# Optimization experiments

Measured on AMD Instinct MI355X. Metric: run time of the kernel, lower is better.

## Reference

```python
import math
import jax, jax.numpy as jnp
import numpy as np

B, H, D, N, M = 4, 8, 64, 8192, 256
EPS = 1e-6


def sample_orthogonal_random_vectors(num_rows, num_cols, seed=0):
    """Faithful port of FavorAttention.sample_orthogonal_random_vectors."""
    rng = np.random.default_rng(seed)
    num_blocks = math.ceil(num_rows / num_cols)
    unstructured = rng.standard_normal((num_blocks, num_cols, num_cols)).astype(np.float32)
    norm = np.linalg.norm(unstructured, axis=-1).reshape(-1, 1)
    q, _ = np.linalg.qr(unstructured)                 # reduced QR per block
    q = np.transpose(q, (0, 2, 1)).reshape(-1, num_cols)
    q = q[:num_rows, :] * norm[:num_rows, :]
    return jnp.asarray(q, dtype=jnp.float32)


def setup_inputs() -> dict:
    key = jax.random.key(0)
    kq, kk, kv = jax.random.split(key, 3)
    return {
        "query": jax.random.normal(kq, (B, H, D, N), dtype=jnp.float32),
        "key": jax.random.normal(kk, (B, H, D, N), dtype=jnp.float32),
        "value": jax.random.normal(kv, (B, H, D, N), dtype=jnp.float32),
        "projection_matrix": sample_orthogonal_random_vectors(M, D),
    }


def randomized_kernel(x, proj, is_query, eps=EPS):
    """FAVOR+ positive softmax features. x: [B,H,D,N] -> phi: [B,H,M,N]."""
    d = x.shape[2]
    data_normalizer = d ** -0.25
    ratio = proj.shape[0] ** -0.5
    # projected: [B,H,M,N]
    u = jnp.einsum('md,bhdn->bhmn', proj, x) * data_normalizer
    # ||x||^2 / (2*sqrt(d)) per token: [B,H,1,N]
    diag = jnp.sum(x * x, axis=2, keepdims=True) * (data_normalizer ** 2) * 0.5
    if is_query:
        stab = jnp.max(u, axis=2, keepdims=True)            # per-token max over features
    else:
        stab = jnp.max(u, axis=(2, 3), keepdims=True)       # global max per (b,h)
    return ratio * (jnp.exp(u - diag - stab) + eps)


def reference(query, key, value, projection_matrix):
    q_phi = randomized_kernel(query, projection_matrix, is_query=True)    # [B,H,M,N]
    k_phi = randomized_kernel(key, projection_matrix, is_query=False)     # [B,H,M,N]
    # kv = key @ value^T over sequence: [B,H,M,D]
    kv = jnp.einsum('bhmn,bhdn->bhmd', k_phi, value)
    key_norm = jnp.sum(k_phi, axis=3)                                     # [B,H,M]
    out = jnp.einsum('bhmn,bhmd->bhnd', q_phi, kv)                        # [B,H,N,D]
    out_norm = jnp.einsum('bhmn,bhm->bhn', q_phi, key_norm)[..., None]    # [B,H,N,1]
    out = out / out_norm
    return jnp.swapaxes(out, 2, 3)                                        # [B,H,D,N]


if __name__ == '__main__':
    o = reference(**setup_inputs())
    print(o.shape, o.dtype)
```

## Files before the change

kernel.cpp:

```cpp
#include <hip/hip_runtime.h>


typedef short s16x8 __attribute__((ext_vector_type(8)));
typedef float f32x4 __attribute__((ext_vector_type(4)));

#define Dv 64
#define Nv 8192
#define Mv 256
#define BHv 32
#define SPL 16
#define NSPL (Nv / SPL)
#define NCH (NSPL / 64)

#define DNRM 0.3535533905932738f
#define EPSV 1e-6f
#define KSTAB 15.0f

#define BARRIER_RAW()                                        \
    do {                                                     \
        asm volatile("s_waitcnt lgkmcnt(0)" ::: "memory");   \
        __builtin_amdgcn_s_barrier();                        \
        __builtin_amdgcn_sched_barrier(0);                   \
    } while (0)

#define OFF_SD 0
#define OFF_T (OFF_SD + BHv * Dv)
#define OFF_SGM (OFF_T + BHv)
#define OFF_SVP (OFF_SGM + BHv * SPL * 4)
#define OFF_KNP (OFF_SVP + BHv * SPL * 64)
#define OFF_KNF (OFF_KNP + BHv * SPL * Mv)
#define OFF_KVP (OFF_KNF + BHv * Mv)
#define OFF_KVT (OFF_KVP + BHv * SPL * Mv * Dv)
#define ZERO_FLOATS (OFF_SGM)

__device__ __forceinline__ unsigned short f2b(float x) {
    return __builtin_bit_cast(unsigned short, (__bf16)x);
}

__device__ __forceinline__ s16x8 load_pfrag(const float* __restrict__ proj, int m,
                                            int kc, int q) {
    const float* p = proj + m * 64 + kc * 32 + q * 8;
    s16x8 r;
#pragma unroll
    for (int j = 0; j < 8; ++j) r[j] = (short)f2b(p[j]);
    return r;
}

__global__ __launch_bounds__(256, 2) void favor_kv(const float* __restrict__ key,
                                                   const float* __restrict__ value,
                                                   const float* __restrict__ proj,
                                                   float* __restrict__ ws) {
    __shared__ __align__(16) unsigned short KT[64][72];
    __shared__ __align__(16) unsigned short VL[64][72];
    __shared__ __align__(16) unsigned short PH[256][40];
    __shared__ __align__(16) float dred[16][64];
    __shared__ __align__(16) float dgl[64];
    const int tid = threadIdx.x;
    const int w = tid >> 6, l = tid & 63, c = l & 15, q = l >> 4;
    const int g = tid >> 4, cs = tid & 15;
    const int s = blockIdx.x, bh = blockIdx.y;
    const float* kp = key + (size_t)bh * Dv * Nv;
    const float* vp = value + (size_t)bh * Dv * Nv;

    s16x8 P[4][2];
#pragma unroll
    for (int mt = 0; mt < 4; ++mt)
#pragma unroll
        for (int kc = 0; kc < 2; ++kc)
            P[mt][kc] = load_pfrag(proj, (4 * w + mt) * 16 + c, kc, q);

    f32x4 kva[4][4];
#pragma unroll
    for (int mt = 0; mt < 4; ++mt)
#pragma unroll
        for (int dt = 0; dt < 4; ++dt) kva[mt][dt] = (f32x4){0.f, 0.f, 0.f, 0.f};
    float kn[4] = {0.f, 0.f, 0.f, 0.f};
    float sv[4] = {0.f, 0.f, 0.f, 0.f};
    float tmax = -3.0e38f;

    float4 kk[4], vv[4];
    {
        const int n0 = s * NSPL;
#pragma unroll
        for (int di = 0; di < 4; ++di) {
            kk[di] = *(const float4*)&kp[(4 * g + di) * Nv + n0 + 4 * cs];
            vv[di] = *(const float4*)&vp[(4 * g + di) * Nv + n0 + 4 * cs];
        }
    }

    for (int ch = 0; ch < NCH; ++ch) {
        if (ch) BARRIER_RAW();
#pragma unroll
        for (int j = 0; j < 4; ++j) {
            const float k0 = ((const float*)&kk[0])[j];
            const float k1 = ((const float*)&kk[1])[j];
            const float k2 = ((const float*)&kk[2])[j];
            const float k3 = ((const float*)&kk[3])[j];
            *(short4*)&KT[4 * cs + j][4 * g] =
                make_short4((short)f2b(k0), (short)f2b(k1), (short)f2b(k2),
                            (short)f2b(k3));
            dred[g][4 * cs + j] = (k0 * k0 + k1 * k1) + (k2 * k2 + k3 * k3);
        }
#pragma unroll
        for (int di = 0; di < 4; ++di) {
            *(short4*)&VL[4 * g + di][4 * cs] = make_short4(
                (short)f2b(vv[di].x), (short)f2b(vv[di].y),
                (short)f2b(vv[di].z), (short)f2b(vv[di].w));
            sv[di] += (vv[di].x + vv[di].y) + (vv[di].z + vv[di].w);
        }
        if (ch + 1 < NCH) {
            const int n1 = s * NSPL + (ch + 1) * 64;
#pragma unroll
            for (int di = 0; di < 4; ++di) {
                kk[di] = *(const float4*)&kp[(4 * g + di) * Nv + n1 + 4 * cs];
                vv[di] = *(const float4*)&vp[(4 * g + di) * Nv + n1 + 4 * cs];
            }
        }
        BARRIER_RAW();
        if (tid < 64) {
            float ds = 0.f;
#pragma unroll
            for (int gg = 0; gg < 16; ++gg) ds += dred[gg][tid];
            dgl[tid] = ds * 0.0625f + KSTAB;
        }
        BARRIER_RAW();
#pragma unroll
        for (int h = 0; h < 2; ++h) {
#pragma unroll
            for (int nt2 = 0; nt2 < 2; ++nt2) {
                const int nt = 2 * h + nt2;
                const s16x8 a0 = *(const s16x8*)&KT[nt * 16 + c][q * 8];
                const s16x8 a1 = *(const s16x8*)&KT[nt * 16 + c][32 + q * 8];
                const float4 dg = *(const float4*)&dgl[nt * 16 + q * 4];
#pragma unroll
                for (int mt = 0; mt < 4; ++mt) {
                    f32x4 u = {0.f, 0.f, 0.f, 0.f};
                    u = __builtin_amdgcn_mfma_f32_16x16x32_bf16(a0, P[mt][0], u, 0, 0, 0);
                    u = __builtin_amdgcn_mfma_f32_16x16x32_bf16(a1, P[mt][1], u, 0, 0, 0);
                    tmax = fmaxf(tmax, fmaxf(fmaxf(u[0], u[1]), fmaxf(u[2], u[3])));
                    const float e0 = __expf(__builtin_fmaf(u[0], DNRM, -dg.x));
                    const float e1 = __expf(__builtin_fmaf(u[1], DNRM, -dg.y));
                    const float e2 = __expf(__builtin_fmaf(u[2], DNRM, -dg.z));
                    const float e3 = __expf(__builtin_fmaf(u[3], DNRM, -dg.w));
                    kn[mt] += (e0 + e1) + (e2 + e3);
                    *(short4*)&PH[(4 * w + mt) * 16 + c][nt2 * 16 + q * 4] =
                        make_short4((short)f2b(e0), (short)f2b(e1),
                                    (short)f2b(e2), (short)f2b(e3));
                }
            }
            s16x8 bf[4];
#pragma unroll
            for (int dt = 0; dt < 4; ++dt)
                bf[dt] = *(const s16x8*)&VL[dt * 16 + c][h * 32 + q * 8];
#pragma unroll
            for (int mt = 0; mt < 4; ++mt) {
                const s16x8 a = *(const s16x8*)&PH[(4 * w + mt) * 16 + c][q * 8];
#pragma unroll
                for (int dt = 0; dt < 4; ++dt)
                    kva[mt][dt] = __builtin_amdgcn_mfma_f32_16x16x32_bf16(
                        a, bf[dt], kva[mt][dt], 0, 0, 0);
            }
        }
    }
#pragma unroll
    for (int off = 1; off < 64; off <<= 1)
        tmax = fmaxf(tmax, __shfl_xor(tmax, off, 64));
    if (l == 0) ws[OFF_SGM + (bh * SPL + s) * 4 + w] = tmax * DNRM;
    float* kvp = ws + OFF_KVP + (size_t)(bh * SPL + s) * Mv * Dv;
#pragma unroll
    for (int mt = 0; mt < 4; ++mt) {
        const int mrow = (4 * w + mt) * 16 + 4 * q;
#pragma unroll
        for (int dt = 0; dt < 4; ++dt) {
            const int dcol = dt * 16 + c;
#pragma unroll
            for (int r = 0; r < 4; ++r)
                kvp[(size_t)(mrow + r) * Dv + dcol] = kva[mt][dt][r];
        }
    }
#pragma unroll
    for (int mt = 0; mt < 4; ++mt) {
        kn[mt] += __shfl_xor(kn[mt], 16, 64);
        kn[mt] += __shfl_xor(kn[mt], 32, 64);
    }
    if (q == 0) {
        float* knp = ws + OFF_KNP + (bh * SPL + s) * Mv;
#pragma unroll
        for (int mt = 0; mt < 4; ++mt) knp[(4 * w + mt) * 16 + c] = kn[mt];
    }
    __syncthreads();
    float* sp = &dred[0][0];
#pragma unroll
    for (int di = 0; di < 4; ++di) sp[(4 * g + di) * 16 + cs] = sv[di];
    __syncthreads();
    if (tid < 64) {
        float t2 = 0.f;
#pragma unroll
        for (int j = 0; j < 16; ++j) t2 += sp[tid * 16 + j];
        ws[OFF_SVP + (bh * SPL + s) * 64 + tid] = t2;
    }
}

__global__ __launch_bounds__(256) void favor_kvred(float* __restrict__ ws) {
    __shared__ float sAl;
    __shared__ float svl[64];
    const int t = threadIdx.x, f = blockIdx.x, bh = blockIdx.y;
    const int flat = f * 1024 + t * 4;
    const int m = flat >> 6, d0 = flat & 63;
    if (t < 64) {
        float v = ws[OFF_SGM + bh * 64 + t];
#pragma unroll
        for (int off = 1; off < 64; off <<= 1)
            v = fmaxf(v, __shfl_xor(v, off, 64));
        if (t == 0) sAl = __expf(KSTAB - v);
    } else if (t < 128) {
        const int d = t - 64;
        float x = 0.f;
#pragma unroll
        for (int s2 = 0; s2 < SPL; ++s2)
            x += ws[OFF_SVP + (bh * SPL + s2) * 64 + d];
        svl[d] = x;
    }
    __syncthreads();
    const float al = sAl;
    float4 acc = make_float4(0.f, 0.f, 0.f, 0.f);
    for (int s2 = 0; s2 < SPL; ++s2) {
        const float4 v =
            *(const float4*)&ws[OFF_KVP + ((size_t)(bh * SPL + s2) << 14) + flat];
        acc.x += v.x; acc.y += v.y; acc.z += v.z; acc.w += v.w;
    }
    acc.x = acc.x * al + EPSV * svl[d0 + 0];
    acc.y = acc.y * al + EPSV * svl[d0 + 1];
    acc.z = acc.z * al + EPSV * svl[d0 + 2];
    acc.w = acc.w * al + EPSV * svl[d0 + 3];
    unsigned short* kvT = (unsigned short*)(ws + OFF_KVT);
    kvT[(bh * 64 + d0 + 0) * 256 + m] = f2b(acc.x);
    kvT[(bh * 64 + d0 + 1) * 256 + m] = f2b(acc.y);
    kvT[(bh * 64 + d0 + 2) * 256 + m] = f2b(acc.z);
    kvT[(bh * 64 + d0 + 3) * 256 + m] = f2b(acc.w);
    atomicAdd(&ws[OFF_SD + bh * 64 + d0 + 0], acc.x);
    atomicAdd(&ws[OFF_SD + bh * 64 + d0 + 1], acc.y);
    atomicAdd(&ws[OFF_SD + bh * 64 + d0 + 2], acc.z);
    atomicAdd(&ws[OFF_SD + bh * 64 + d0 + 3], acc.w);
    if (t < 16) {
        const int mm = f * 16 + t;
        float kk = 0.f;
        for (int s2 = 0; s2 < SPL; ++s2)
            kk += ws[OFF_KNP + (bh * SPL + s2) * Mv + mm];
        const float knf = kk * al + EPSV * (float)Nv;
        ws[OFF_KNF + bh * Mv + mm] = knf;
        atomicAdd(&ws[OFF_T + bh], knf);
    }
}

__global__ __launch_bounds__(256, 2) void favor_out(const float* __restrict__ query,
                                                    const float* __restrict__ proj,
                                                    const float* __restrict__ ws,
                                                    float* __restrict__ out) {
    __shared__ __align__(16) unsigned short PHT[64][264];
    __shared__ __align__(16) unsigned short KVL[64][264];
    __shared__ float npart[4][64];
    __shared__ float knl[256];
    __shared__ float cw[4][64];
    __shared__ float dql[64];
    __shared__ float Sl[64];
    __shared__ float Ts;
    unsigned short (*QT)[72] = (unsigned short (*)[72]) & PHT[0][0];
    float (*dred)[64] = (float (*)[64])((char*)&PHT[0][0] + 9216);
    const int tid = threadIdx.x;
    const int w = tid >> 6, l = tid & 63, c = l & 15, q = l >> 4;
    const int g = tid >> 4, cs = tid & 15;
    const int nb = blockIdx.x, bh = blockIdx.y;
    const int n0 = nb * 64;
    const float* qp = query + (size_t)bh * Dv * Nv;
    const uint4* kvg = (const uint4*)((const unsigned short*)(ws + OFF_KVT) +
                                      (size_t)bh * 64 * 256);

    float4 qq[4];
#pragma unroll
    for (int di = 0; di < 4; ++di)
        qq[di] = *(const float4*)&qp[(4 * g + di) * Nv + n0 + 4 * cs];
    uint4 kvr[8];
#pragma unroll
    for (int i = 0; i < 8; ++i) kvr[i] = kvg[i * 256 + tid];

#pragma unroll
    for (int j = 0; j < 4; ++j) {
        const float v0 = ((const float*)&qq[0])[j];
        const float v1 = ((const float*)&qq[1])[j];
        const float v2 = ((const float*)&qq[2])[j];
        const float v3 = ((const float*)&qq[3])[j];
        *(short4*)&QT[4 * cs + j][4 * g] =
            make_short4((short)f2b(v0), (short)f2b(v1), (short)f2b(v2),
                        (short)f2b(v3));
        dred[g][4 * cs + j] = (v0 * v0 + v1 * v1) + (v2 * v2 + v3 * v3);
    }
#pragma unroll
    for (int i = 0; i < 8; ++i) {
        const int j = i * 256 + tid;
        *(uint4*)&KVL[j >> 5][(j & 31) * 8] = kvr[i];
    }
    knl[tid] = ws[OFF_KNF + bh * Mv + tid];
    if (tid < 64) Sl[tid] = ws[OFF_SD + bh * 64 + tid];
    if (tid == 0) Ts = ws[OFF_T + bh];

    s16x8 P[4][2];
#pragma unroll
    for (int mt = 0; mt < 4; ++mt)
#pragma unroll
        for (int kc = 0; kc < 2; ++kc)
            P[mt][kc] = load_pfrag(proj, (4 * w + mt) * 16 + c, kc, q);
    __syncthreads();

    if (tid < 64) {
        float dsum = 0.f;
#pragma unroll
        for (int gg = 0; gg < 16; ++gg) dsum += dred[gg][tid];
        dql[tid] = dsum * 0.0625f;
    }
    float knr[4][4];
#pragma unroll
    for (int mt = 0; mt < 4; ++mt) {
        const int mb = (4 * w + mt) * 16 + 4 * q;
#pragma unroll
        for (int r = 0; r < 4; ++r) knr[mt][r] = knl[mb + r];
    }

    f32x4 u[4][4];
#pragma unroll
    for (int mt = 0; mt < 4; ++mt)
#pragma unroll
        for (int nt = 0; nt < 4; ++nt) u[mt][nt] = (f32x4){0.f, 0.f, 0.f, 0.f};
#pragma unroll
    for (int nt = 0; nt < 4; ++nt) {
        const s16x8 b0 = *(const s16x8*)&QT[nt * 16 + c][q * 8];
        const s16x8 b1 = *(const s16x8*)&QT[nt * 16 + c][32 + q * 8];
#pragma unroll
        for (int mt = 0; mt < 4; ++mt) {
            u[mt][nt] =
                __builtin_amdgcn_mfma_f32_16x16x32_bf16(P[mt][0], b0, u[mt][nt], 0, 0, 0);
            u[mt][nt] =
                __builtin_amdgcn_mfma_f32_16x16x32_bf16(P[mt][1], b1, u[mt][nt], 0, 0, 0);
        }
    }
    __syncthreads();
#pragma unroll
    for (int nt = 0; nt < 4; ++nt) {
        const float dq = dql[nt * 16 + c];
        float np = 0.f;
        float vm = -3.4e38f;
#pragma unroll
        for (int mt = 0; mt < 4; ++mt) {
            vm = fmaxf(vm, fmaxf(fmaxf(u[mt][nt][0], u[mt][nt][1]),
                                 fmaxf(u[mt][nt][2], u[mt][nt][3])));
            const float e0 = __expf(__builtin_fmaf(u[mt][nt][0], DNRM, -dq));
            const float e1 = __expf(__builtin_fmaf(u[mt][nt][1], DNRM, -dq));
            const float e2 = __expf(__builtin_fmaf(u[mt][nt][2], DNRM, -dq));
            const float e3 = __expf(__builtin_fmaf(u[mt][nt][3], DNRM, -dq));
            const int mb = (4 * w + mt) * 16 + 4 * q;
            np += e0 * knr[mt][0] + e1 * knr[mt][1] + e2 * knr[mt][2] +
                  e3 * knr[mt][3];
            *(short4*)&PHT[nt * 16 + c][mb] = make_short4(
                (short)f2b(e0), (short)f2b(e1), (short)f2b(e2), (short)f2b(e3));
        }
        np += __shfl_xor(np, 16, 64);
        np += __shfl_xor(np, 32, 64);
        vm = fmaxf(vm, __shfl_xor(vm, 16, 64));
        vm = fmaxf(vm, __shfl_xor(vm, 32, 64));
        if (q == 0) {
            npart[w][nt * 16 + c] = np;
            cw[w][nt * 16 + c] = vm;
        }
    }
    __syncthreads();
    f32x4 acc[4];
#pragma unroll
    for (int dt = 0; dt < 4; ++dt) acc[dt] = (f32x4){0.f, 0.f, 0.f, 0.f};
#pragma unroll
    for (int kc = 0; kc < 8; ++kc) {
        const s16x8 a = *(const s16x8*)&PHT[w * 16 + c][kc * 32 + q * 8];
#pragma unroll
        for (int dt = 0; dt < 4; ++dt) {
            const s16x8 b = *(const s16x8*)&KVL[dt * 16 + c][kc * 32 + q * 8];
            acc[dt] = __builtin_amdgcn_mfma_f32_16x16x32_bf16(a, b, acc[dt], 0, 0, 0);
        }
    }
    __syncthreads();
    float* ot = (float*)&PHT[0][0];
    float rn[4], gm[4];
#pragma unroll
    for (int r = 0; r < 4; ++r) {
        const int nl = w * 16 + 4 * q + r;
        const float npsum = (npart[0][nl] + npart[1][nl]) +
                            (npart[2][nl] + npart[3][nl]);
        const float st =
            fmaxf(fmaxf(cw[0][nl], cw[1][nl]), fmaxf(cw[2][nl], cw[3][nl]));
        const float gamma = EPSV * __expf(st * DNRM);
        gm[r] = gamma;
        rn[r] = 1.0f / (npsum + gamma * Ts);
    }
#pragma unroll
    for (int dt = 0; dt < 4; ++dt)
#pragma unroll
        for (int r = 0; r < 4; ++r)
            ot[(dt * 16 + c) * 68 + (w * 16 + 4 * q + r)] =
                (acc[dt][r] + gm[r] * Sl[dt * 16 + c]) * rn[r];
    __syncthreads();
    float* op = out + (size_t)bh * Dv * Nv;
    {
        const int d = tid >> 2, ng = (tid & 3) * 16;
#pragma unroll
        for (int i = 0; i < 4; ++i) {
            const float4 v = *(const float4*)&ot[d * 68 + ng + i * 4];
            *(float4*)&op[d * Nv + n0 + ng + i * 4] = v;
        }
    }
}

extern "C" void kernel_launch(void* const* d_in, const int* in_sizes, int n_in,
                              void* d_out, int out_size, void* d_ws, size_t ws_size,
                              hipStream_t stream) {
    const float* q = (const float*)d_in[0];
    const float* k = (const float*)d_in[1];
    const float* v = (const float*)d_in[2];
    const float* proj = (const float*)d_in[3];
    float* ws = (float*)d_ws;
    float* out = (float*)d_out;

    hipMemsetAsync(ws, 0, (size_t)ZERO_FLOATS * sizeof(float), stream);
    favor_kv<<<dim3(SPL, 32), 256, 0, stream>>>(k, v, proj, ws);
    favor_kvred<<<dim3(16, 32), 256, 0, stream>>>(ws);
    favor_out<<<dim3(Nv / 64, 32), 256, 0, stream>>>(q, proj, ws, out);
}
```

Baseline: 324.8 us.

## Process two token tiles per output block and drop memset and atomics

The output kernel now covers 128 tokens per block in two passes. This amortizes the staging of the bf16 kv matrix, the key norms and the projection fragments, and prefetches the second query tile early. The column sums of kv and the total key norm are now recomputed in each block from the staged data, which removes the global atomics and the workspace memset launch. The cost is fewer blocks (half the grid), a serial 256-element sum in a few threads, and Sl now being a sum of bf16-rounded values.

```diff
diff --git a/kernel.cpp b/kernel.cpp
--- a/kernel.cpp
+++ b/kernel.cpp
@@ -23,18 +23,19 @@
         __builtin_amdgcn_sched_barrier(0);                   \
     } while (0)
 
-#define OFF_SD 0
-#define OFF_T (OFF_SD + BHv * Dv)
-#define OFF_SGM (OFF_T + BHv)
+#define OFF_SGM 0
 #define OFF_SVP (OFF_SGM + BHv * SPL * 4)
 #define OFF_KNP (OFF_SVP + BHv * SPL * 64)
 #define OFF_KNF (OFF_KNP + BHv * SPL * Mv)
 #define OFF_KVP (OFF_KNF + BHv * Mv)
 #define OFF_KVT (OFF_KVP + BHv * SPL * Mv * Dv)
-#define ZERO_FLOATS (OFF_SGM)
 
 __device__ __forceinline__ unsigned short f2b(float x) {
     return __builtin_bit_cast(unsigned short, (__bf16)x);
+}
+__device__ __forceinline__ float b2f(unsigned short u) {
+    const unsigned int v = ((unsigned int)u) << 16;
+    return __builtin_bit_cast(float, v);
 }
 
 __device__ __forceinline__ s16x8 load_pfrag(const float* __restrict__ proj, int m,
@@ -238,18 +239,12 @@
     kvT[(bh * 64 + d0 + 1) * 256 + m] = f2b(acc.y);
     kvT[(bh * 64 + d0 + 2) * 256 + m] = f2b(acc.z);
     kvT[(bh * 64 + d0 + 3) * 256 + m] = f2b(acc.w);
-    atomicAdd(&ws[OFF_SD + bh * 64 + d0 + 0], acc.x);
-    atomicAdd(&ws[OFF_SD + bh * 64 + d0 + 1], acc.y);
-    atomicAdd(&ws[OFF_SD + bh * 64 + d0 + 2], acc.z);
-    atomicAdd(&ws[OFF_SD + bh * 64 + d0 + 3], acc.w);
     if (t < 16) {
         const int mm = f * 16 + t;
         float kk = 0.f;
         for (int s2 = 0; s2 < SPL; ++s2)
             kk += ws[OFF_KNP + (bh * SPL + s2) * Mv + mm];
-        const float knf = kk * al + EPSV * (float)Nv;
-        ws[OFF_KNF + bh * Mv + mm] = knf;
-        atomicAdd(&ws[OFF_T + bh], knf);
+        ws[OFF_KNF + bh * Mv + mm] = kk * al + EPSV * (float)Nv;
     }
 }
 
@@ -264,32 +259,35 @@
     __shared__ float cw[4][64];
     __shared__ float dql[64];
     __shared__ float Sl[64];
-    __shared__ float Ts;
+    __shared__ float Tsh;
     unsigned short (*QT)[72] = (unsigned short (*)[72]) & PHT[0][0];
     float (*dred)[64] = (float (*)[64])((char*)&PHT[0][0] + 9216);
     const int tid = threadIdx.x;
     const int w = tid >> 6, l = tid & 63, c = l & 15, q = l >> 4;
     const int g = tid >> 4, cs = tid & 15;
     const int nb = blockIdx.x, bh = blockIdx.y;
-    const int n0 = nb * 64;
+    const int n0 = nb * 128;
     const float* qp = query + (size_t)bh * Dv * Nv;
     const uint4* kvg = (const uint4*)((const unsigned short*)(ws + OFF_KVT) +
                                       (size_t)bh * 64 * 256);
 
-    float4 qq[4];
+    float4 qqA[4], qqB[4];
 #pragma unroll
     for (int di = 0; di < 4; ++di)
-        qq[di] = *(const float4*)&qp[(4 * g + di) * Nv + n0 + 4 * cs];
+        qqA[di] = *(const float4*)&qp[(4 * g + di) * Nv + n0 + 4 * cs];
     uint4 kvr[8];
 #pragma unroll
     for (int i = 0; i < 8; ++i) kvr[i] = kvg[i * 256 + tid];
+#pragma unroll
+    for (int di = 0; di < 4; ++di)
+        qqB[di] = *(const float4*)&qp[(4 * g + di) * Nv + n0 + 64 + 4 * cs];
 
 #pragma unroll
     for (int j = 0; j < 4; ++j) {
-        const float v0 = ((const float*)&qq[0])[j];
-        const float v1 = ((const float*)&qq[1])[j];
-        const float v2 = ((const float*)&qq[2])[j];
-        const float v3 = ((const float*)&qq[3])[j];
+        const float v0 = ((const float*)&qqA[0])[j];
+        const float v1 = ((const float*)&qqA[1])[j];
+        const float v2 = ((const float*)&qqA[2])[j];
+        const float v3 = ((const float*)&qqA[3])[j];
         *(short4*)&QT[4 * cs + j][4 * g] =
             make_short4((short)f2b(v0), (short)f2b(v1), (short)f2b(v2),
                         (short)f2b(v3));
@@ -301,8 +299,6 @@
         *(uint4*)&KVL[j >> 5][(j & 31) * 8] = kvr[i];
     }
     knl[tid] = ws[OFF_KNF + bh * Mv + tid];
-    if (tid < 64) Sl[tid] = ws[OFF_SD + bh * 64 + tid];
-    if (tid == 0) Ts = ws[OFF_T + bh];
 
     s16x8 P[4][2];
 #pragma unroll
@@ -310,15 +306,8 @@
 #pragma unroll
         for (int kc = 0; kc < 2; ++kc)
             P[mt][kc] = load_pfrag(proj, (4 * w + mt) * 16 + c, kc, q);
-    __syncthreads();
-
-    if (tid < 64) {
-        float dsum = 0.f;
-#pragma unroll
-        for (int gg = 0; gg < 16; ++gg) dsum += dred[gg][tid];
-        dql[tid] = dsum * 0.0625f;
-    }
     float knr[4][4];
+    BARRIER_RAW();
 #pragma unroll
     for (int mt = 0; mt < 4; ++mt) {
         const int mb = (4 * w + mt) * 16 + 4 * q;
@@ -326,93 +315,129 @@
         for (int r = 0; r < 4; ++r) knr[mt][r] = knl[mb + r];
     }
 
-    f32x4 u[4][4];
-#pragma unroll
-    for (int mt = 0; mt < 4; ++mt)
-#pragma unroll
-        for (int nt = 0; nt < 4; ++nt) u[mt][nt] = (f32x4){0.f, 0.f, 0.f, 0.f};
-#pragma unroll
-    for (int nt = 0; nt < 4; ++nt) {
-        const s16x8 b0 = *(const s16x8*)&QT[nt * 16 + c][q * 8];
-        const s16x8 b1 = *(const s16x8*)&QT[nt * 16 + c][32 + q * 8];
-#pragma unroll
-        for (int mt = 0; mt < 4; ++mt) {
-            u[mt][nt] =
-                __builtin_amdgcn_mfma_f32_16x16x32_bf16(P[mt][0], b0, u[mt][nt], 0, 0, 0);
-            u[mt][nt] =
-                __builtin_amdgcn_mfma_f32_16x16x32_bf16(P[mt][1], b1, u[mt][nt], 0, 0, 0);
-        }
-    }
-    __syncthreads();
-#pragma unroll
-    for (int nt = 0; nt < 4; ++nt) {
-        const float dq = dql[nt * 16 + c];
-        float np = 0.f;
-        float vm = -3.4e38f;
-#pragma unroll
-        for (int mt = 0; mt < 4; ++mt) {
-            vm = fmaxf(vm, fmaxf(fmaxf(u[mt][nt][0], u[mt][nt][1]),
-                                 fmaxf(u[mt][nt][2], u[mt][nt][3])));
-            const float e0 = __expf(__builtin_fmaf(u[mt][nt][0], DNRM, -dq));
-            const float e1 = __expf(__builtin_fmaf(u[mt][nt][1], DNRM, -dq));
-            const float e2 = __expf(__builtin_fmaf(u[mt][nt][2], DNRM, -dq));
-            const float e3 = __expf(__builtin_fmaf(u[mt][nt][3], DNRM, -dq));
-            const int mb = (4 * w + mt) * 16 + 4 * q;
-            np += e0 * knr[mt][0] + e1 * knr[mt][1] + e2 * knr[mt][2] +
-                  e3 * knr[mt][3];
-            *(short4*)&PHT[nt * 16 + c][mb] = make_short4(
-                (short)f2b(e0), (short)f2b(e1), (short)f2b(e2), (short)f2b(e3));
-        }
-        np += __shfl_xor(np, 16, 64);
-        np += __shfl_xor(np, 32, 64);
-        vm = fmaxf(vm, __shfl_xor(vm, 16, 64));
-        vm = fmaxf(vm, __shfl_xor(vm, 32, 64));
-        if (q == 0) {
-            npart[w][nt * 16 + c] = np;
-            cw[w][nt * 16 + c] = vm;
-        }
-    }
-    __syncthreads();
-    f32x4 acc[4];
-#pragma unroll
-    for (int dt = 0; dt < 4; ++dt) acc[dt] = (f32x4){0.f, 0.f, 0.f, 0.f};
-#pragma unroll
-    for (int kc = 0; kc < 8; ++kc) {
-        const s16x8 a = *(const s16x8*)&PHT[w * 16 + c][kc * 32 + q * 8];
-#pragma unroll
-        for (int dt = 0; dt < 4; ++dt) {
-            const s16x8 b = *(const s16x8*)&KVL[dt * 16 + c][kc * 32 + q * 8];
-            acc[dt] = __builtin_amdgcn_mfma_f32_16x16x32_bf16(a, b, acc[dt], 0, 0, 0);
-        }
-    }
-    __syncthreads();
-    float* ot = (float*)&PHT[0][0];
-    float rn[4], gm[4];
-#pragma unroll
-    for (int r = 0; r < 4; ++r) {
-        const int nl = w * 16 + 4 * q + r;
-        const float npsum = (npart[0][nl] + npart[1][nl]) +
-                            (npart[2][nl] + npart[3][nl]);
-        const float st =
-            fmaxf(fmaxf(cw[0][nl], cw[1][nl]), fmaxf(cw[2][nl], cw[3][nl]));
-        const float gamma = EPSV * __expf(st * DNRM);
-        gm[r] = gamma;
-        rn[r] = 1.0f / (npsum + gamma * Ts);
-    }
-#pragma unroll
-    for (int dt = 0; dt < 4; ++dt)
-#pragma unroll
-        for (int r = 0; r < 4; ++r)
-            ot[(dt * 16 + c) * 68 + (w * 16 + 4 * q + r)] =
-                (acc[dt][r] + gm[r] * Sl[dt * 16 + c]) * rn[r];
-    __syncthreads();
     float* op = out + (size_t)bh * Dv * Nv;
-    {
-        const int d = tid >> 2, ng = (tid & 3) * 16;
-#pragma unroll
-        for (int i = 0; i < 4; ++i) {
-            const float4 v = *(const float4*)&ot[d * 68 + ng + i * 4];
-            *(float4*)&op[d * Nv + n0 + ng + i * 4] = v;
+#pragma unroll
+    for (int t = 0; t < 2; ++t) {
+        if (tid < 64) {
+            float dsum = 0.f;
+#pragma unroll
+            for (int gg = 0; gg < 16; ++gg) dsum += dred[gg][tid];
+            dql[tid] = dsum * 0.0625f;
+        } else if (t == 0 && tid < 128) {
+            const int d = tid - 64;
+            float ssum = 0.f;
+#pragma unroll
+            for (int m2 = 0; m2 < 256; ++m2) ssum += b2f(KVL[d][m2]);
+            Sl[d] = ssum;
+        } else if (t == 0 && tid == 128) {
+            float tsum = 0.f;
+#pragma unroll
+            for (int m2 = 0; m2 < 256; ++m2) tsum += knl[m2];
+            Tsh = tsum;
+        }
+        f32x4 u[4][4];
+#pragma unroll
+        for (int mt = 0; mt < 4; ++mt)
+#pragma unroll
+            for (int nt = 0; nt < 4; ++nt) u[mt][nt] = (f32x4){0.f, 0.f, 0.f, 0.f};
+#pragma unroll
+        for (int nt = 0; nt < 4; ++nt) {
+            const s16x8 b0 = *(const s16x8*)&QT[nt * 16 + c][q * 8];
+            const s16x8 b1 = *(const s16x8*)&QT[nt * 16 + c][32 + q * 8];
+#pragma unroll
+            for (int mt = 0; mt < 4; ++mt) {
+                u[mt][nt] = __builtin_amdgcn_mfma_f32_16x16x32_bf16(P[mt][0], b0,
+                                                                    u[mt][nt], 0, 0, 0);
+                u[mt][nt] = __builtin_amdgcn_mfma_f32_16x16x32_bf16(P[mt][1], b1,
+                                                                    u[mt][nt], 0, 0, 0);
+            }
+        }
+        BARRIER_RAW();
+#pragma unroll
+        for (int nt = 0; nt < 4; ++nt) {
+            const float dq = dql[nt * 16 + c];
+            float np = 0.f;
+            float vm = -3.4e38f;
+#pragma unroll
+            for (int mt = 0; mt < 4; ++mt) {
+                vm = fmaxf(vm, fmaxf(fmaxf(u[mt][nt][0], u[mt][nt][1]),
+                                     fmaxf(u[mt][nt][2], u[mt][nt][3])));
+                const float e0 = __expf(__builtin_fmaf(u[mt][nt][0], DNRM, -dq));
+                const float e1 = __expf(__builtin_fmaf(u[mt][nt][1], DNRM, -dq));
+                const float e2 = __expf(__builtin_fmaf(u[mt][nt][2], DNRM, -dq));
+                const float e3 = __expf(__builtin_fmaf(u[mt][nt][3], DNRM, -dq));
+                const int mb = (4 * w + mt) * 16 + 4 * q;
+                np += e0 * knr[mt][0] + e1 * knr[mt][1] + e2 * knr[mt][2] +
+                      e3 * knr[mt][3];
+                *(short4*)&PHT[nt * 16 + c][mb] = make_short4(
+                    (short)f2b(e0), (short)f2b(e1), (short)f2b(e2), (short)f2b(e3));
+            }
+            np += __shfl_xor(np, 16, 64);
+            np += __shfl_xor(np, 32, 64);
+            vm = fmaxf(vm, __shfl_xor(vm, 16, 64));
+            vm = fmaxf(vm, __shfl_xor(vm, 32, 64));
+            if (q == 0) {
+                npart[w][nt * 16 + c] = np;
+                cw[w][nt * 16 + c] = vm;
+            }
+        }
+        BARRIER_RAW();
+        f32x4 acc[4];
+#pragma unroll
+        for (int dt = 0; dt < 4; ++dt) acc[dt] = (f32x4){0.f, 0.f, 0.f, 0.f};
+#pragma unroll
+        for (int kc = 0; kc < 8; ++kc) {
+            const s16x8 a = *(const s16x8*)&PHT[w * 16 + c][kc * 32 + q * 8];
+#pragma unroll
+            for (int dt = 0; dt < 4; ++dt) {
+                const s16x8 b = *(const s16x8*)&KVL[dt * 16 + c][kc * 32 + q * 8];
+                acc[dt] =
+                    __builtin_amdgcn_mfma_f32_16x16x32_bf16(a, b, acc[dt], 0, 0, 0);
+            }
+        }
+        BARRIER_RAW();
+        float* ot = (float*)&PHT[0][0];
+        float rn[4], gm[4];
+#pragma unroll
+        for (int r = 0; r < 4; ++r) {
+            const int nl = w * 16 + 4 * q + r;
+            const float npsum = (npart[0][nl] + npart[1][nl]) +
+                                (npart[2][nl] + npart[3][nl]);
+            const float st =
+                fmaxf(fmaxf(cw[0][nl], cw[1][nl]), fmaxf(cw[2][nl], cw[3][nl]));
+            const float gamma = EPSV * __expf(st * DNRM);
+            gm[r] = gamma;
+            rn[r] = 1.0f / (npsum + gamma * Tsh);
+        }
+#pragma unroll
+        for (int dt = 0; dt < 4; ++dt)
+#pragma unroll
+            for (int r = 0; r < 4; ++r)
+                ot[(dt * 16 + c) * 68 + (w * 16 + 4 * q + r)] =
+                    (acc[dt][r] + gm[r] * Sl[dt * 16 + c]) * rn[r];
+        BARRIER_RAW();
+        {
+            const int d = tid >> 2, ng = (tid & 3) * 16;
+#pragma unroll
+            for (int i = 0; i < 4; ++i) {
+                const float4 v = *(const float4*)&ot[d * 68 + ng + i * 4];
+                *(float4*)&op[d * Nv + n0 + t * 64 + ng + i * 4] = v;
+            }
+        }
+        if (t == 0) {
+            BARRIER_RAW();
+#pragma unroll
+            for (int j = 0; j < 4; ++j) {
+                const float v0 = ((const float*)&qqB[0])[j];
+                const float v1 = ((const float*)&qqB[1])[j];
+                const float v2 = ((const float*)&qqB[2])[j];
+                const float v3 = ((const float*)&qqB[3])[j];
+                *(short4*)&QT[4 * cs + j][4 * g] =
+                    make_short4((short)f2b(v0), (short)f2b(v1), (short)f2b(v2),
+                                (short)f2b(v3));
+                dred[g][4 * cs + j] = (v0 * v0 + v1 * v1) + (v2 * v2 + v3 * v3);
+            }
+            BARRIER_RAW();
         }
     }
 }
@@ -427,8 +452,7 @@
     float* ws = (float*)d_ws;
     float* out = (float*)d_out;
 
-    hipMemsetAsync(ws, 0, (size_t)ZERO_FLOATS * sizeof(float), stream);
     favor_kv<<<dim3(SPL, 32), 256, 0, stream>>>(k, v, proj, ws);
     favor_kvred<<<dim3(16, 32), 256, 0, stream>>>(ws);
-    favor_out<<<dim3(Nv / 64, 32), 256, 0, stream>>>(q, proj, ws, out);
-}
+    favor_out<<<dim3(Nv / 128, 32), 256, 0, stream>>>(q, proj, ws, out);
+}
```

New measurement: 280.0 us. 13.8% less time.
